# Kernel optimization log

Measured on AMD Instinct MI355X. Metric: run time of the kernel, lower is better.

Reference implementation:

```python
import jax, jax.numpy as jnp
import numpy as np

EPS = 1e-06


def _feature_map(x):
    # elu(x) + 1  (elu with alpha=1)
    return jnp.where(x > 0, x + 1.0, jnp.exp(x))


def setup_inputs() -> dict:
    key = jax.random.key(0)
    k1, k2, k3 = jax.random.split(key, 3)
    N, L, S, H, D = 4, 8192, 8192, 8, 64
    q = jax.random.normal(k1, (N, L, H, D), dtype=jnp.float32)
    k = jax.random.normal(k2, (N, S, H, D), dtype=jnp.float32)
    v = jax.random.normal(k3, (N, S, H, D), dtype=jnp.float32)
    q_mask = jnp.ones((N, L), dtype=jnp.float32)
    kv_mask = jnp.ones((N, S), dtype=jnp.float32)
    return {"q": q, "k": k, "v": v, "q_mask": q_mask, "kv_mask": kv_mask}


def reference(q, k, v, q_mask, kv_mask):
    # Linear attention with elu+1 feature map (Katharopoulos et al.)
    qf = _feature_map(q)  # [N, L, H, D]
    kf = _feature_map(k)  # [N, S, H, D]
    qf = q_mask[:, :, None, None] * qf
    kf = kv_mask[:, :, None, None] * kf
    vm = kv_mask[:, :, None, None] * v
    S = v.shape[1]
    # global KV state: [N, H, D, Dv]; v scaled by 1/S for numerical stability
    kv = jnp.einsum('nshd,nshv->nhdv', kf, vm / S)
    # normalizer: einsum('nlhd,nshd->nlh') == q . sum_s(k)
    k_sum = kf.sum(axis=1)  # [N, H, D]
    div = 1.0 / (jnp.einsum('nlhd,nhd->nlh', qf, k_sum) + EPS)
    out = S * jnp.einsum('nlhd,nhdv,nlh->nlhv', qf, kv, div)
    return out
```

## Files before the change

### kernel.cpp

```cpp
#include <hip/hip_runtime.h>
#include <math.h>


#define EPS 1e-6f

static constexpr int Nc = 4;
static constexpr int Lc = 8192;
static constexpr int Sc = 8192;
static constexpr int Hc = 8;
static constexpr int NH = Nc * Hc;
static constexpr int STATE = 64 * 64 + 64;
static constexpr int TS = 32;
static constexpr int TSP = 36;
static constexpr int LDSTR = 68;

typedef __attribute__((ext_vector_type(4))) short short4v;
typedef __attribute__((ext_vector_type(8))) short short8v;
typedef __attribute__((ext_vector_type(4))) float f32x4;

__device__ __forceinline__ float fmap(float x) {
    return x > 0.f ? x + 1.f : __expf(x);
}
__device__ __forceinline__ unsigned short f2bf(float x) {
    unsigned int u = __float_as_uint(x);
    u += 0x7FFFu + ((u >> 16) & 1u);
    return (unsigned short)(u >> 16);
}
__device__ __forceinline__ float bf2f(unsigned short h) {
    return __uint_as_float(((unsigned int)h) << 16);
}
__device__ __forceinline__ short8v ld8(const unsigned short* p) {
    short4v a = *(const short4v*)p;
    short4v b = *(const short4v*)(p + 4);
    return __builtin_shufflevector(a, b, 0, 1, 2, 3, 4, 5, 6, 7);
}

__global__ __launch_bounds__(256, 4) void k1_partial(
    const float* __restrict__ kg, const float* __restrict__ vg,
    const float* __restrict__ kv_mask,
    float* __restrict__ partial, int chunks, int sc)
{
    __shared__ unsigned short kTh[64][TSP], kTl[64][TSP];
    __shared__ unsigned short vTh[64][TSP], vTl[64][TSP];
    __shared__ float ksb[16][64];

    const int bid = blockIdx.x;
    const int pair = bid / chunks;
    const int chunk = bid - pair * chunks;
    const int n = pair >> 3;
    const int h = pair & 7;
    const int s0 = chunk * sc;
    const int t = threadIdx.x;
    const int g = t >> 4;
    const int c4 = (t & 15) * 4;
    const int lane = t & 63;
    const int wv = t >> 6;
    const int row16 = lane & 15;
    const int g8 = (lane >> 4) * 8;

    f32x4 acc[4] = {{0.f,0.f,0.f,0.f},{0.f,0.f,0.f,0.f},
                    {0.f,0.f,0.f,0.f},{0.f,0.f,0.f,0.f}};
    float ksm[4] = {0.f, 0.f, 0.f, 0.f};

    const size_t rowstride = (size_t)Hc * 64;
    const size_t gbase = ((size_t)n * Sc * Hc + h) * 64 + c4;
    const int mbase = n * Sc;

    float4 kp0, kp1, vp0, vp1;
    float mpe, mpo;

    {
        const int s = s0 + 2 * g;
        const size_t be = gbase + (size_t)s * rowstride;
        kp0 = *(const float4*)(kg + be);
        kp1 = *(const float4*)(kg + be + rowstride);
        vp0 = *(const float4*)(vg + be);
        vp1 = *(const float4*)(vg + be + rowstride);
        mpe = kv_mask[mbase + s];
        mpo = kv_mask[mbase + s + 1];
    }

    for (int sb = 0; sb < sc; sb += TS) {
        const float4 ck0 = kp0, ck1 = kp1, cv0 = vp0, cv1 = vp1;
        const float cme = mpe, cmo = mpo;

        {
            const int nxt = (sb + TS < sc) ? sb + TS : sb;
            const int s = s0 + nxt + 2 * g;
            const size_t be = gbase + (size_t)s * rowstride;
            kp0 = *(const float4*)(kg + be);
            kp1 = *(const float4*)(kg + be + rowstride);
            vp0 = *(const float4*)(vg + be);
            vp1 = *(const float4*)(vg + be + rowstride);
            mpe = kv_mask[mbase + s];
            mpo = kv_mask[mbase + s + 1];
        }

        const float* kep = &ck0.x;
        const float* kop = &ck1.x;
        const float* vep = &cv0.x;
        const float* vop = &cv1.x;
        #pragma unroll
        for (int j = 0; j < 4; ++j) {
            const float fe = cme * fmap(kep[j]);
            const float fo = cmo * fmap(kop[j]);
            ksm[j] += fe + fo;
            const unsigned short he = f2bf(fe), ho = f2bf(fo);
            const unsigned short le = f2bf(fe - bf2f(he)), lo_ = f2bf(fo - bf2f(ho));
            *(unsigned int*)&kTh[c4 + j][2 * g] = (unsigned)he | ((unsigned)ho << 16);
            *(unsigned int*)&kTl[c4 + j][2 * g] = (unsigned)le | ((unsigned)lo_ << 16);
            const float ue = cme * vep[j];
            const float uo = cmo * vop[j];
            const unsigned short vhe = f2bf(ue), vho = f2bf(uo);
            const unsigned short vle = f2bf(ue - bf2f(vhe)), vlo = f2bf(uo - bf2f(vho));
            *(unsigned int*)&vTh[c4 + j][2 * g] = (unsigned)vhe | ((unsigned)vho << 16);
            *(unsigned int*)&vTl[c4 + j][2 * g] = (unsigned)vle | ((unsigned)vlo << 16);
        }
        __syncthreads();

        const short8v Ah = ld8(&kTh[wv * 16 + row16][g8]);
        const short8v Al = ld8(&kTl[wv * 16 + row16][g8]);
        #pragma unroll
        for (int bt = 0; bt < 4; ++bt) {
            const short8v Bh = ld8(&vTh[bt * 16 + row16][g8]);
            const short8v Bl = ld8(&vTl[bt * 16 + row16][g8]);
            acc[bt] = __builtin_amdgcn_mfma_f32_16x16x32_bf16(Ah, Bh, acc[bt], 0, 0, 0);
            acc[bt] = __builtin_amdgcn_mfma_f32_16x16x32_bf16(Al, Bh, acc[bt], 0, 0, 0);
            acc[bt] = __builtin_amdgcn_mfma_f32_16x16x32_bf16(Ah, Bl, acc[bt], 0, 0, 0);
        }
        __syncthreads();
    }

    float* outp = partial + (size_t)bid * STATE;
    #pragma unroll
    for (int bt = 0; bt < 4; ++bt) {
        #pragma unroll
        for (int r = 0; r < 4; ++r) {
            outp[(size_t)(wv * 16 + (lane >> 4) * 4 + r) * 64 + bt * 16 + (lane & 15)]
                = acc[bt][r];
        }
    }

    *(f32x4*)&ksb[g][c4] = (f32x4){ksm[0], ksm[1], ksm[2], ksm[3]};
    __syncthreads();
    if (t < 64) {
        float s = 0.f;
        #pragma unroll
        for (int i = 0; i < 16; ++i) s += ksb[i][t];
        outp[4096 + t] = s;
    }
}

__global__ __launch_bounds__(256) void k2_reduce(
    const float* __restrict__ src, float* __restrict__ dst, int nred)
{
    const int p = blockIdx.x / 5;
    const int seg = blockIdx.x - p * 5;
    const int e4 = seg * 256 + threadIdx.x;
    if (e4 >= STATE / 4) return;
    const float4* s = (const float4*)(src + (size_t)p * nred * STATE) + e4;
    float4 acc = make_float4(0.f, 0.f, 0.f, 0.f);
    #pragma unroll 4
    for (int j = 0; j < nred; ++j) {
        float4 x = s[(size_t)j * (STATE / 4)];
        acc.x += x.x; acc.y += x.y; acc.z += x.z; acc.w += x.w;
    }
    ((float4*)(dst + (size_t)p * STATE))[e4] = acc;
}

__global__ __launch_bounds__(256, 4) void k3_out(
    const float* __restrict__ qg, const float* __restrict__ state,
    const float* __restrict__ q_mask, float* __restrict__ outg)
{
    __shared__ float qf[64][LDSTR];
    __shared__ float kvs[64][64];
    __shared__ float ksum[64];
    __shared__ float dinv[64];

    const int nblk = Lc / 64;
    const int bid = blockIdx.x;
    const int pair = bid / nblk;
    const int lblk = bid - pair * nblk;
    const int n = pair / Hc;
    const int h = pair - n * Hc;
    const int l0 = lblk * 64;
    const int t = threadIdx.x;

    const float* st = state + (size_t)pair * STATE;
    #pragma unroll
    for (int i = 0; i < 4; ++i)
        ((float4*)kvs)[t + i * 256] = ((const float4*)st)[t + i * 256];
    if (t < 16)
        ((float4*)ksum)[t] = *((const float4*)(st + 4096) + t);
    __syncthreads();

    #pragma unroll
    for (int p = 0; p < 4; ++p) {
        const int f = t + p * 256;
        const int row = f >> 4;
        const int c4 = (f & 15) * 4;
        const int l = l0 + row;
        const size_t base = ((size_t)(n * Lc + l) * Hc + h) * 64 + c4;
        const float4 qq = *(const float4*)(qg + base);
        const float m = q_mask[n * Lc + l];
        float4 q4;
        q4.x = m * fmap(qq.x); q4.y = m * fmap(qq.y);
        q4.z = m * fmap(qq.z); q4.w = m * fmap(qq.w);
        *(float4*)&qf[row][c4] = q4;
        const float4 ks4 = *(const float4*)&ksum[c4];
        float dp = q4.x * ks4.x + q4.y * ks4.y + q4.z * ks4.z + q4.w * ks4.w;
        dp += __shfl_xor(dp, 1);
        dp += __shfl_xor(dp, 2);
        dp += __shfl_xor(dp, 4);
        dp += __shfl_xor(dp, 8);
        if ((t & 15) == 0) dinv[row] = 1.0f / (dp + EPS);
    }
    __syncthreads();

    const int r0 = (t >> 4) * 4;
    const int c0 = (t & 15) * 4;
    float acc[4][4] = {};
    #pragma unroll
    for (int k4 = 0; k4 < 64; k4 += 4) {
        float a[4][4], b[4][4];
        #pragma unroll
        for (int i = 0; i < 4; ++i)
            *(float4*)a[i] = *(const float4*)&qf[r0 + i][k4];
        #pragma unroll
        for (int kk = 0; kk < 4; ++kk)
            *(float4*)b[kk] = *(const float4*)&kvs[k4 + kk][c0];
        #pragma unroll
        for (int i = 0; i < 4; ++i)
            #pragma unroll
            for (int j = 0; j < 4; ++j)
                #pragma unroll
                for (int kk = 0; kk < 4; ++kk)
                    acc[i][j] += a[i][kk] * b[kk][j];
    }

    #pragma unroll
    for (int i = 0; i < 4; ++i) {
        const float di = dinv[r0 + i];
        float4 o = make_float4(acc[i][0] * di, acc[i][1] * di,
                               acc[i][2] * di, acc[i][3] * di);
        const size_t base = ((size_t)(n * Lc + l0 + r0 + i) * Hc + h) * 64 + c0;
        *(float4*)(outg + base) = o;
    }
}

extern "C" void kernel_launch(void* const* d_in, const int* in_sizes, int n_in,
                              void* d_out, int out_size, void* d_ws, size_t ws_size,
                              hipStream_t stream)
{
    (void)in_sizes; (void)n_in; (void)out_size;
    const float* q       = (const float*)d_in[0];
    const float* k       = (const float*)d_in[1];
    const float* v       = (const float*)d_in[2];
    const float* q_mask  = (const float*)d_in[3];
    const float* kv_mask = (const float*)d_in[4];
    float* out = (float*)d_out;

    const size_t stBytes  = (size_t)STATE * sizeof(float);
    const size_t finBytes = (size_t)NH * stBytes;
    const size_t p2Bytes  = (size_t)NH * 4 * stBytes;

    float* fin = (float*)d_ws;
    float* p2  = (float*)((char*)d_ws + finBytes);
    float* p1  = (float*)((char*)d_ws + finBytes + p2Bytes);

    int chunks = 0;
    for (int c = 64; c >= 8; c >>= 1) {
        if (ws_size >= finBytes + p2Bytes + (size_t)NH * c * stBytes) { chunks = c; break; }
    }

    if (chunks >= 8) {
        k1_partial<<<NH * chunks, 256, 0, stream>>>(k, v, kv_mask, p1, chunks, Sc / chunks);
        k2_reduce<<<NH * 4 * 5, 256, 0, stream>>>(p1, p2, chunks / 4);
        k2_reduce<<<NH * 5, 256, 0, stream>>>(p2, fin, 4);
    } else {
        k1_partial<<<NH, 256, 0, stream>>>(k, v, kv_mask, fin, 1, Sc);
    }

    k3_out<<<NH * (Lc / 64), 256, 0, stream>>>(q, fin, q_mask, out);
}
```

Before: 90.56 us.

## Use split-bf16 MFMA in output kernel with pretransposed bf16 KV state

The output kernel's FP32 FMA 64x64x64 matmul is replaced by MFMA bf16 instructions using a hi/lo split (three products) to keep near-FP32 accuracy. A new finalize kernel reduces the partial states and writes the KV state transposed and pre-split into bf16 hi/lo words, so the output kernel can load it directly into LDS. Results are staged through LDS so global stores stay coalesced. k1's launch bound is raised to 8 waves per SIMD, and the split adds conversion work in exchange for cheaper matrix math.

```diff
diff --git a/kernel.cpp b/kernel.cpp
--- a/kernel.cpp
+++ b/kernel.cpp
@@ -12,7 +12,7 @@
 static constexpr int STATE = 64 * 64 + 64;
 static constexpr int TS = 32;
 static constexpr int TSP = 36;
-static constexpr int LDSTR = 68;
+static constexpr int QSP = 68;
 
 typedef __attribute__((ext_vector_type(4))) short short4v;
 typedef __attribute__((ext_vector_type(8))) short short8v;
@@ -34,8 +34,11 @@
     short4v b = *(const short4v*)(p + 4);
     return __builtin_shufflevector(a, b, 0, 1, 2, 3, 4, 5, 6, 7);
 }
-
-__global__ __launch_bounds__(256, 4) void k1_partial(
+__device__ __forceinline__ unsigned int pack2(unsigned short a, unsigned short b) {
+    return (unsigned)a | ((unsigned)b << 16);
+}
+
+__global__ __launch_bounds__(256, 8) void k1_partial(
     const float* __restrict__ kg, const float* __restrict__ vg,
     const float* __restrict__ kv_mask,
     float* __restrict__ partial, int chunks, int sc)
@@ -107,14 +110,14 @@
             ksm[j] += fe + fo;
             const unsigned short he = f2bf(fe), ho = f2bf(fo);
             const unsigned short le = f2bf(fe - bf2f(he)), lo_ = f2bf(fo - bf2f(ho));
-            *(unsigned int*)&kTh[c4 + j][2 * g] = (unsigned)he | ((unsigned)ho << 16);
-            *(unsigned int*)&kTl[c4 + j][2 * g] = (unsigned)le | ((unsigned)lo_ << 16);
+            *(unsigned int*)&kTh[c4 + j][2 * g] = pack2(he, ho);
+            *(unsigned int*)&kTl[c4 + j][2 * g] = pack2(le, lo_);
             const float ue = cme * vep[j];
             const float uo = cmo * vop[j];
             const unsigned short vhe = f2bf(ue), vho = f2bf(uo);
             const unsigned short vle = f2bf(ue - bf2f(vhe)), vlo = f2bf(uo - bf2f(vho));
-            *(unsigned int*)&vTh[c4 + j][2 * g] = (unsigned)vhe | ((unsigned)vho << 16);
-            *(unsigned int*)&vTl[c4 + j][2 * g] = (unsigned)vle | ((unsigned)vlo << 16);
+            *(unsigned int*)&vTh[c4 + j][2 * g] = pack2(vhe, vho);
+            *(unsigned int*)&vTl[c4 + j][2 * g] = pack2(vle, vlo);
         }
         __syncthreads();
 
@@ -168,12 +171,57 @@
     ((float4*)(dst + (size_t)p * STATE))[e4] = acc;
 }
 
+__global__ __launch_bounds__(256) void k2b_finalize(
+    const float* __restrict__ src, float* __restrict__ dst, int nred)
+{
+    __shared__ float kv[64][QSP];
+    __shared__ float kss[64];
+
+    const int pair = blockIdx.x;
+    const int t = threadIdx.x;
+    const float4* sbase = (const float4*)(src + (size_t)pair * nred * STATE);
+
+    #pragma unroll
+    for (int i = 0; i < 4; ++i) {
+        const int e4 = t + i * 256;
+        float4 a = make_float4(0.f, 0.f, 0.f, 0.f);
+        for (int j = 0; j < nred; ++j) {
+            float4 x = sbase[(size_t)j * (STATE / 4) + e4];
+            a.x += x.x; a.y += x.y; a.z += x.z; a.w += x.w;
+        }
+        *(float4*)&kv[e4 >> 4][(e4 & 15) * 4] = a;
+    }
+    if (t < 16) {
+        float4 a = make_float4(0.f, 0.f, 0.f, 0.f);
+        for (int j = 0; j < nred; ++j) {
+            float4 x = sbase[(size_t)j * (STATE / 4) + 1024 + t];
+            a.x += x.x; a.y += x.y; a.z += x.z; a.w += x.w;
+        }
+        *(float4*)&kss[t * 4] = a;
+    }
+    __syncthreads();
+
+    unsigned int* dw = (unsigned int*)(dst + (size_t)pair * STATE);
+    #pragma unroll
+    for (int i = 0; i < 8; ++i) {
+        const int w = t + i * 256;
+        const int dv = w >> 5;
+        const int d0 = (w & 31) * 2;
+        const float f0 = kv[d0][dv];
+        const float f1 = kv[d0 + 1][dv];
+        const unsigned short h0 = f2bf(f0), h1 = f2bf(f1);
+        dw[w] = pack2(h0, h1);
+        dw[2048 + w] = pack2(f2bf(f0 - bf2f(h0)), f2bf(f1 - bf2f(h1)));
+    }
+    if (t < 64) dst[(size_t)pair * STATE + 4096 + t] = kss[t];
+}
+
 __global__ __launch_bounds__(256, 4) void k3_out(
     const float* __restrict__ qg, const float* __restrict__ state,
     const float* __restrict__ q_mask, float* __restrict__ outg)
 {
-    __shared__ float qf[64][LDSTR];
-    __shared__ float kvs[64][64];
+    __shared__ __align__(16) unsigned short qsp[2][64][QSP];
+    __shared__ unsigned short kvt[2][64][QSP];
     __shared__ float ksum[64];
     __shared__ float dinv[64];
 
@@ -181,17 +229,25 @@
     const int bid = blockIdx.x;
     const int pair = bid / nblk;
     const int lblk = bid - pair * nblk;
-    const int n = pair / Hc;
-    const int h = pair - n * Hc;
+    const int n = pair >> 3;
+    const int h = pair & 7;
     const int l0 = lblk * 64;
     const int t = threadIdx.x;
-
-    const float* st = state + (size_t)pair * STATE;
-    #pragma unroll
-    for (int i = 0; i < 4; ++i)
-        ((float4*)kvs)[t + i * 256] = ((const float4*)st)[t + i * 256];
-    if (t < 16)
-        ((float4*)ksum)[t] = *((const float4*)(st + 4096) + t);
+    const int lane = t & 63;
+    const int wv = t >> 6;
+    const int row16 = lane & 15;
+    const int g8 = (lane >> 4) * 8;
+
+    const unsigned int* sw = (const unsigned int*)(state + (size_t)pair * STATE);
+    #pragma unroll
+    for (int i = 0; i < 8; ++i) {
+        const int w = t + i * 256;
+        const int dv = w >> 5;
+        const int d2 = (w & 31) * 2;
+        *(unsigned int*)&kvt[0][dv][d2] = sw[w];
+        *(unsigned int*)&kvt[1][dv][d2] = sw[2048 + w];
+    }
+    if (t < 64) ksum[t] = ((const float*)state)[(size_t)pair * STATE + 4096 + t];
     __syncthreads();
 
     #pragma unroll
@@ -203,12 +259,14 @@
         const size_t base = ((size_t)(n * Lc + l) * Hc + h) * 64 + c4;
         const float4 qq = *(const float4*)(qg + base);
         const float m = q_mask[n * Lc + l];
-        float4 q4;
-        q4.x = m * fmap(qq.x); q4.y = m * fmap(qq.y);
-        q4.z = m * fmap(qq.z); q4.w = m * fmap(qq.w);
-        *(float4*)&qf[row][c4] = q4;
-        const float4 ks4 = *(const float4*)&ksum[c4];
-        float dp = q4.x * ks4.x + q4.y * ks4.y + q4.z * ks4.z + q4.w * ks4.w;
+        const float q0 = m * fmap(qq.x), q1 = m * fmap(qq.y);
+        const float q2 = m * fmap(qq.z), q3 = m * fmap(qq.w);
+        const unsigned short h0 = f2bf(q0), h1 = f2bf(q1), h2 = f2bf(q2), h3 = f2bf(q3);
+        *(unsigned int*)&qsp[0][row][c4]     = pack2(h0, h1);
+        *(unsigned int*)&qsp[0][row][c4 + 2] = pack2(h2, h3);
+        *(unsigned int*)&qsp[1][row][c4]     = pack2(f2bf(q0 - bf2f(h0)), f2bf(q1 - bf2f(h1)));
+        *(unsigned int*)&qsp[1][row][c4 + 2] = pack2(f2bf(q2 - bf2f(h2)), f2bf(q3 - bf2f(h3)));
+        float dp = q0 * ksum[c4] + q1 * ksum[c4 + 1] + q2 * ksum[c4 + 2] + q3 * ksum[c4 + 3];
         dp += __shfl_xor(dp, 1);
         dp += __shfl_xor(dp, 2);
         dp += __shfl_xor(dp, 4);
@@ -217,34 +275,41 @@
     }
     __syncthreads();
 
-    const int r0 = (t >> 4) * 4;
-    const int c0 = (t & 15) * 4;
-    float acc[4][4] = {};
-    #pragma unroll
-    for (int k4 = 0; k4 < 64; k4 += 4) {
-        float a[4][4], b[4][4];
-        #pragma unroll
-        for (int i = 0; i < 4; ++i)
-            *(float4*)a[i] = *(const float4*)&qf[r0 + i][k4];
-        #pragma unroll
-        for (int kk = 0; kk < 4; ++kk)
-            *(float4*)b[kk] = *(const float4*)&kvs[k4 + kk][c0];
-        #pragma unroll
-        for (int i = 0; i < 4; ++i)
-            #pragma unroll
-            for (int j = 0; j < 4; ++j)
-                #pragma unroll
-                for (int kk = 0; kk < 4; ++kk)
-                    acc[i][j] += a[i][kk] * b[kk][j];
-    }
-
-    #pragma unroll
-    for (int i = 0; i < 4; ++i) {
-        const float di = dinv[r0 + i];
-        float4 o = make_float4(acc[i][0] * di, acc[i][1] * di,
-                               acc[i][2] * di, acc[i][3] * di);
-        const size_t base = ((size_t)(n * Lc + l0 + r0 + i) * Hc + h) * 64 + c0;
-        *(float4*)(outg + base) = o;
+    f32x4 acc[4] = {{0.f,0.f,0.f,0.f},{0.f,0.f,0.f,0.f},
+                    {0.f,0.f,0.f,0.f},{0.f,0.f,0.f,0.f}};
+    #pragma unroll
+    for (int ks = 0; ks < 2; ++ks) {
+        const short8v Ah = ld8(&qsp[0][wv * 16 + row16][ks * 32 + g8]);
+        const short8v Al = ld8(&qsp[1][wv * 16 + row16][ks * 32 + g8]);
+        #pragma unroll
+        for (int bt = 0; bt < 4; ++bt) {
+            const short8v Bh = ld8(&kvt[0][bt * 16 + row16][ks * 32 + g8]);
+            const short8v Bl = ld8(&kvt[1][bt * 16 + row16][ks * 32 + g8]);
+            acc[bt] = __builtin_amdgcn_mfma_f32_16x16x32_bf16(Ah, Bh, acc[bt], 0, 0, 0);
+            acc[bt] = __builtin_amdgcn_mfma_f32_16x16x32_bf16(Al, Bh, acc[bt], 0, 0, 0);
+            acc[bt] = __builtin_amdgcn_mfma_f32_16x16x32_bf16(Ah, Bl, acc[bt], 0, 0, 0);
+        }
+    }
+    __syncthreads();
+
+    float (*outs)[QSP] = reinterpret_cast<float (*)[QSP]>(&qsp[0][0][0]);
+    #pragma unroll
+    for (int bt = 0; bt < 4; ++bt) {
+        #pragma unroll
+        for (int r = 0; r < 4; ++r) {
+            const int row = wv * 16 + (lane >> 4) * 4 + r;
+            outs[row][bt * 16 + row16] = acc[bt][r] * dinv[row];
+        }
+    }
+    __syncthreads();
+
+    #pragma unroll
+    for (int p = 0; p < 4; ++p) {
+        const int f = t + p * 256;
+        const int row = f >> 4;
+        const int c4 = (f & 15) * 4;
+        const size_t base = ((size_t)(n * Lc + l0 + row) * Hc + h) * 64 + c4;
+        *(float4*)(outg + base) = *(const float4*)&outs[row][c4];
     }
 }
 
@@ -276,9 +341,11 @@
     if (chunks >= 8) {
         k1_partial<<<NH * chunks, 256, 0, stream>>>(k, v, kv_mask, p1, chunks, Sc / chunks);
         k2_reduce<<<NH * 4 * 5, 256, 0, stream>>>(p1, p2, chunks / 4);
-        k2_reduce<<<NH * 5, 256, 0, stream>>>(p2, fin, 4);
+        k2b_finalize<<<NH, 256, 0, stream>>>(p2, fin, 4);
     } else {
-        k1_partial<<<NH, 256, 0, stream>>>(k, v, kv_mask, fin, 1, Sc);
+        float* p1fb = (float*)((char*)d_ws + finBytes);
+        k1_partial<<<NH, 256, 0, stream>>>(k, v, kv_mask, p1fb, 1, Sc);
+        k2b_finalize<<<NH, 256, 0, stream>>>(p1fb, fin, 1);
     }
 
     k3_out<<<NH * (Lc / 64), 256, 0, stream>>>(q, fin, q_mask, out);
```

Result: faster. 86.06 us (-5.0%).
